# Kernel tuning notes

Measured on AMD Instinct MI355X. Metric: run time of the kernel, lower is better.

The kernel has to match this reference:

```python
import jax, jax.numpy as jnp
import numpy as np

B, L, D = 2, 2048, 1024
H = 16
DH = D // H
FACTOR = 0.6
U = max(1, min(L, int(FACTOR * L)))  # 1228 selected queries


def setup_inputs() -> dict:
    key = jax.random.key(0)
    ks = jax.random.split(key, 9)
    s = 0.02
    return {
        "x": jax.random.normal(ks[0], (B, L, D), dtype=jnp.float32),
        "Wq": jax.random.normal(ks[1], (D, D), dtype=jnp.float32) * s,
        "bq": jnp.zeros((D,), dtype=jnp.float32),
        "Wk": jax.random.normal(ks[2], (D, D), dtype=jnp.float32) * s,
        "bk": jnp.zeros((D,), dtype=jnp.float32),
        "Wv": jax.random.normal(ks[3], (D, D), dtype=jnp.float32) * s,
        "bv": jnp.zeros((D,), dtype=jnp.float32),
        "Wo": jax.random.normal(ks[4], (D, D), dtype=jnp.float32) * s,
        "bo": jnp.zeros((D,), dtype=jnp.float32),
    }


def _split_heads(x):
    b, l, d = x.shape
    return x.reshape(b, l, H, DH).transpose(0, 2, 1, 3)  # [b,h,l,dh]


def reference(x, Wq, bq, Wk, bk, Wv, bv, Wo, bo):
    b, l, _ = x.shape
    scale = 1.0 / jnp.sqrt(jnp.asarray(DH, dtype=x.dtype))

    q = _split_heads(x @ Wq + bq)  # [b,h,l,dh]
    k = _split_heads(x @ Wk + bk)
    v = _split_heads(x @ Wv + bv)

    # full scores for sparsity heuristic
    scores = jnp.einsum("bhqd,bhkd->bhqk", q, k) * scale  # [b,h,l,l]
    sparsity = scores.max(axis=-1) - scores.mean(axis=-1)  # [b,h,l]

    _, top_idx = jax.lax.top_k(sparsity, U)  # [b,h,U]

    # gather selected queries, attend only on those rows
    q_sel = jnp.take_along_axis(q, top_idx[..., None], axis=2)  # [b,h,U,dh]
    scores_sel = jnp.einsum("bhud,bhkd->bhuk", q_sel, k) * scale  # [b,h,U,l]
    attn = jax.nn.softmax(scores_sel, axis=-1)
    out_sel = jnp.einsum("bhuk,bhkd->bhud", attn, v)  # [b,h,U,dh]

    # scatter back into zero-initialized output
    bi = jnp.arange(b)[:, None, None]
    hi = jnp.arange(H)[None, :, None]
    out = jnp.zeros_like(q).at[bi, hi, top_idx].set(out_sel)  # [b,h,l,dh]

    out = out.transpose(0, 2, 1, 3).reshape(b, l, D)
    return out @ Wo + bo
```

## Files before the change

kernel.cpp:

```cpp
#include <hip/hip_runtime.h>
#include <math.h>
#include <stdint.h>

#define Bn 2
#define Ln 2048
#define Dn 1024
#define Hn 16
#define DHn 64
#define Un 1228
#define BHn (Bn*Hn)
#define SCALE 0.125f
#define WIN 32
#define WHALF 16
#define SXf 16.0f
#define SWf 256.0f
#define SQf 16.0f
#define SVf 16.0f
#define SPf 16.0f
#define ESC_PROJ (1.0f / 4096.0f)
#define ESC_OUT  (1.0f / 65536.0f)
#define PSC (SCALE / 256.0f)
#define QPS 88

typedef _Float16 f16;
typedef __attribute__((ext_vector_type(8))) _Float16 f16x8;
typedef __attribute__((ext_vector_type(4))) float f32x4;
struct h4s { f16 x, y, z, w; };

__device__ __forceinline__ void splitf16(float f, f16& hi, f16& lo) {
  hi = (f16)f;
  lo = (f16)(f - (float)hi);
}

__device__ __forceinline__ void gl_lds16(const void* g, void* l) {
  __builtin_amdgcn_global_load_lds(
      (const __attribute__((address_space(1))) void*)g,
      (__attribute__((address_space(3))) void*)l, 16, 0, 0);
}

#define MFMA(a, b, c) __builtin_amdgcn_mfma_f32_16x16x32_f16((a), (b), (c), 0, 0, 0)

__global__ __launch_bounds__(256) void split_kernel(
    const float* __restrict__ in, f16* __restrict__ oh, f16* __restrict__ ol, int n4) {
  int i = blockIdx.x * 256 + threadIdx.x;
  if (i >= n4) return;
  float4 v = ((const float4*)in)[i];
  h4s h, l;
  splitf16(v.x * SXf, h.x, l.x); splitf16(v.y * SXf, h.y, l.y);
  splitf16(v.z * SXf, h.z, l.z); splitf16(v.w * SXf, h.w, l.w);
  ((h4s*)oh)[i] = h; ((h4s*)ol)[i] = l;
}

__global__ __launch_bounds__(256) void tsplit_w4(
    const float* __restrict__ W0, const float* __restrict__ W1,
    const float* __restrict__ W2, const float* __restrict__ W3,
    f16* __restrict__ oh, f16* __restrict__ ol) {
  __shared__ float ts[64][65];
  const int t = threadIdx.x;
  const int r0 = blockIdx.x * 64, c0 = blockIdx.y * 64;
  const int z = blockIdx.z;
  const float* in = (z == 0) ? W0 : (z == 1) ? W1 : (z == 2) ? W2 : W3;
#pragma unroll
  for (int c = 0; c < 4; ++c) {
    int f = (c * 256 + t) * 4; int row = f >> 6, col = f & 63;
    float4 v = *(const float4*)&in[(size_t)(r0 + row) * Dn + c0 + col];
    ts[row][col] = v.x; ts[row][col + 1] = v.y; ts[row][col + 2] = v.z; ts[row][col + 3] = v.w;
  }
  __syncthreads();
#pragma unroll
  for (int c = 0; c < 4; ++c) {
    int f = (c * 256 + t) * 4; int crow = f >> 6, rcol = f & 63;
    h4s h, l;
    splitf16(ts[rcol + 0][crow] * SWf, h.x, l.x);
    splitf16(ts[rcol + 1][crow] * SWf, h.y, l.y);
    splitf16(ts[rcol + 2][crow] * SWf, h.z, l.z);
    splitf16(ts[rcol + 3][crow] * SWf, h.w, l.w);
    size_t o = (size_t)(z * 1024 + c0 + crow) * Dn + r0 + rcol;
    *(h4s*)&oh[o] = h; *(h4s*)&ol[o] = l;
  }
}

__global__ void gemm_qkv(
    const f16* __restrict__ Ah, const f16* __restrict__ Al,
    const f16* __restrict__ Bth, const f16* __restrict__ Btl,
    const float* __restrict__ bq, const float* __restrict__ bk, const float* __restrict__ bv,
    float* __restrict__ Qf, f16* __restrict__ Qbh,
    float* __restrict__ Kf, f16* __restrict__ Kbh,
    f16* __restrict__ Vh16, int K) {
  __shared__ f16 sAh[128 * 32], sAl[128 * 32], sBh[128 * 32], sBl[128 * 32];
  const int t = threadIdx.x;
  const int w = t >> 6, lane = t & 63, lm = lane & 15, q = lane >> 4;
  const int wr = w >> 1, wc = w & 1;
  const int n0 = blockIdx.x * 128, m0 = blockIdx.y * 128;
  f32x4 acc[4][4] = {};
  for (int k0 = 0; k0 < K; k0 += 32) {
    const f16* s0 = Ah + (size_t)m0 * K + k0;
    const f16* s1 = Al + (size_t)m0 * K + k0;
    const f16* s2 = Bth + (size_t)n0 * K + k0;
    const f16* s3 = Btl + (size_t)n0 * K + k0;
#pragma unroll
    for (int c = 0; c < 2; ++c) {
      int f = (c * 256 + t) * 8; int row = f >> 5, col = f & 31;
      size_t go = (size_t)row * K + col;
      gl_lds16(s0 + go, &sAh[f]);
      gl_lds16(s1 + go, &sAl[f]);
      gl_lds16(s2 + go, &sBh[f]);
      gl_lds16(s3 + go, &sBl[f]);
    }
    __syncthreads();
    f16x8 a_h[4], a_l[4], b_h[4], b_l[4];
#pragma unroll
    for (int mi = 0; mi < 4; ++mi) {
      int r = (wr * 64 + mi * 16 + lm) * 32 + q * 8;
      a_h[mi] = *(const f16x8*)&sAh[r];
      a_l[mi] = *(const f16x8*)&sAl[r];
    }
#pragma unroll
    for (int ni = 0; ni < 4; ++ni) {
      int r = (wc * 64 + ni * 16 + lm) * 32 + q * 8;
      b_h[ni] = *(const f16x8*)&sBh[r];
      b_l[ni] = *(const f16x8*)&sBl[r];
    }
#pragma unroll
    for (int mi = 0; mi < 4; ++mi)
#pragma unroll
      for (int ni = 0; ni < 4; ++ni) {
        acc[mi][ni] = MFMA(a_h[mi], b_h[ni], acc[mi][ni]);
        acc[mi][ni] = MFMA(a_h[mi], b_l[ni], acc[mi][ni]);
        acc[mi][ni] = MFMA(a_l[mi], b_h[ni], acc[mi][ni]);
      }
    __syncthreads();
  }
#pragma unroll
  for (int mi = 0; mi < 4; ++mi)
#pragma unroll
    for (int ni = 0; ni < 4; ++ni) {
      int nglob = n0 + wc * 64 + ni * 16;
      int seg = nglob >> 10;
      int c = (nglob & 1023) + lm;
      const float* bp = (seg == 0) ? bq : (seg == 1) ? bk : bv;
      float bvv = bp[c];
#pragma unroll
      for (int r = 0; r < 4; ++r) {
        int grow = m0 + wr * 64 + mi * 16 + q * 4 + r;
        float v = acc[mi][ni][r] * ESC_PROJ + bvv;
        size_t o = (size_t)grow * 1024 + c;
        if (seg == 0) {
          Qf[o] = v;
          Qbh[o] = (f16)(v * SQf);
        } else if (seg == 1) {
          Kf[o] = v;
          Kbh[o] = (f16)(v * SQf);
        } else {
          Vh16[o] = (f16)(v * SVf);
        }
      }
    }
}

__global__ __launch_bounds__(256) void tsplit_v(
    const f16* __restrict__ Vh16, f16* __restrict__ out) {
  __shared__ f16 ts[64][72];
  const int t = threadIdx.x;
  const int l0 = blockIdx.x * 64;
  const int bh = blockIdx.y, b = bh >> 4, h = bh & 15;
#pragma unroll
  for (int c = 0; c < 2; ++c) {
    int e = c * 256 + t; int row = e >> 3, cg = e & 7;
    *(uint4*)&ts[row][cg * 8] =
        *(const uint4*)&Vh16[((size_t)b * Ln + l0 + row) * Dn + h * DHn + cg * 8];
  }
  __syncthreads();
#pragma unroll
  for (int c = 0; c < 2; ++c) {
    int e = c * 256 + t; int drow = e >> 3, lg = e & 7;
    f16 tmp[8];
#pragma unroll
    for (int j = 0; j < 8; ++j) tmp[j] = ts[lg * 8 + j][drow];
    *(uint4*)&out[((size_t)bh * DHn + drow) * Ln + l0 + lg * 8] = *(uint4*)tmp;
  }
}

__global__ __launch_bounds__(256, 4) void gemm_a1(
    const f16* __restrict__ A,
    const f16* __restrict__ Bth, const f16* __restrict__ Btl,
    const float* __restrict__ bias, float escale,
    float* __restrict__ Cf, int M, int N, int K) {
  __shared__ f16 sA[128 * 32], sBh[64 * 32], sBl[64 * 32];
  const int t = threadIdx.x;
  const int w = t >> 6, lane = t & 63, lm = lane & 15, q = lane >> 4;
  const int wr = w >> 1, wc = w & 1;
  const int n0 = blockIdx.x * 64, m0 = blockIdx.y * 128;
  f32x4 acc[4][2] = {};
  for (int k0 = 0; k0 < K; k0 += 32) {
    const f16* s0 = A + (size_t)m0 * K + k0;
    const f16* s2 = Bth + (size_t)n0 * K + k0;
    const f16* s3 = Btl + (size_t)n0 * K + k0;
#pragma unroll
    for (int c = 0; c < 2; ++c) {
      int f = (c * 256 + t) * 8; int row = f >> 5, col = f & 31;
      gl_lds16(s0 + (size_t)row * K + col, &sA[f]);
    }
    {
      int f = t * 8; int row = f >> 5, col = f & 31;
      gl_lds16(s2 + (size_t)row * K + col, &sBh[f]);
      gl_lds16(s3 + (size_t)row * K + col, &sBl[f]);
    }
    __syncthreads();
    f16x8 a_[4], b_h[2], b_l[2];
#pragma unroll
    for (int mi = 0; mi < 4; ++mi)
      a_[mi] = *(const f16x8*)&sA[(wr * 64 + mi * 16 + lm) * 32 + q * 8];
#pragma unroll
    for (int ni = 0; ni < 2; ++ni) {
      int r = (wc * 32 + ni * 16 + lm) * 32 + q * 8;
      b_h[ni] = *(const f16x8*)&sBh[r];
      b_l[ni] = *(const f16x8*)&sBl[r];
    }
#pragma unroll
    for (int mi = 0; mi < 4; ++mi)
#pragma unroll
      for (int ni = 0; ni < 2; ++ni) {
        acc[mi][ni] = MFMA(a_[mi], b_h[ni], acc[mi][ni]);
        acc[mi][ni] = MFMA(a_[mi], b_l[ni], acc[mi][ni]);
      }
    __syncthreads();
  }
#pragma unroll
  for (int mi = 0; mi < 4; ++mi)
#pragma unroll
    for (int ni = 0; ni < 2; ++ni) {
      int gcol = n0 + wc * 32 + ni * 16 + lm;
      float bvv = bias[gcol];
#pragma unroll
      for (int r = 0; r < 4; ++r) {
        int grow = m0 + wr * 64 + mi * 16 + q * 4 + r;
        Cf[(size_t)grow * N + gcol] = acc[mi][ni][r] * escale + bvv;
      }
    }
}

__global__ __launch_bounds__(256) void ksum_part(
    const f16* __restrict__ Kh, float* __restrict__ ksum) {
  __shared__ float red[4][64];
  const int t = threadIdx.x, d = t & 63, seg = t >> 6;
  const int bx = blockIdx.x, bh = blockIdx.y, b = bh >> 4, h = bh & 15;
  float s = 0.f;
  const int lbase = bx * 256 + seg * 64;
  for (int r = 0; r < 64; ++r) {
    size_t o = ((size_t)b * Ln + lbase + r) * Dn + h * DHn + d;
    s += (float)Kh[o];
  }
  red[seg][d] = s;
  __syncthreads();
  if (t < 64) atomicAdd(&ksum[bh * DHn + t], red[0][t] + red[1][t] + red[2][t] + red[3][t]);
}

__global__ __launch_bounds__(256, 2) void attn_stats_mfma(
    const f16* __restrict__ Qh, const f16* __restrict__ Kh,
    const float* __restrict__ ksum,
    float* __restrict__ row_max, float* __restrict__ spars) {
  __shared__ f16 sQh[128 * 64], sKh[128 * 64];
  __shared__ float redm[128][5];
  const int t = threadIdx.x;
  const int w = t >> 6, lane = t & 63, lm = lane & 15, q = lane >> 4;
  const int bh = blockIdx.y, b = bh >> 4, h = bh & 15;
  const int q0 = blockIdx.x * 128;
  const f16* qsh = Qh + ((size_t)b * Ln + q0) * Dn + h * DHn;
#pragma unroll
  for (int c = 0; c < 4; ++c) {
    int f = (c * 256 + t) * 8; int row = f >> 6, c16 = (f >> 3) & 7;
    size_t go = (size_t)row * Dn + ((c16 ^ (row & 7)) << 3);
    gl_lds16(qsh + go, &sQh[f]);
  }
  __syncthreads();
  f16x8 a_h[8][2];
#pragma unroll
  for (int mi = 0; mi < 8; ++mi)
#pragma unroll
    for (int ks = 0; ks < 2; ++ks) {
      int row = mi * 16 + lm;
      int r = row * 64 + (((ks * 4 + q) ^ (row & 7)) << 3);
      a_h[mi][ks] = *(const f16x8*)&sQh[r];
    }
  float rmax[8][4];
#pragma unroll
  for (int mi = 0; mi < 8; ++mi)
#pragma unroll
    for (int r = 0; r < 4; ++r) rmax[mi][r] = -1e30f;

  for (int kt = 0; kt < Ln / 128; ++kt) {
    __syncthreads();
    const f16* ksh = Kh + ((size_t)b * Ln + kt * 128) * Dn + h * DHn;
#pragma unroll
    for (int c = 0; c < 4; ++c) {
      int f = (c * 256 + t) * 8; int row = f >> 6, c16 = (f >> 3) & 7;
      size_t go = (size_t)row * Dn + ((c16 ^ (row & 7)) << 3);
      gl_lds16(ksh + go, &sKh[f]);
    }
    __syncthreads();
#pragma unroll
    for (int ni = 0; ni < 2; ++ni) {
      int bcol = (w * 2 + ni) * 16;
      f16x8 b_h[2];
#pragma unroll
      for (int ks = 0; ks < 2; ++ks) {
        int row = bcol + lm;
        int r = row * 64 + (((ks * 4 + q) ^ (row & 7)) << 3);
        b_h[ks] = *(const f16x8*)&sKh[r];
      }
#pragma unroll
      for (int mi = 0; mi < 8; ++mi) {
        f32x4 acc = {0.f, 0.f, 0.f, 0.f};
        __builtin_amdgcn_s_setprio(1);
        acc = MFMA(a_h[mi][0], b_h[0], acc);
        acc = MFMA(a_h[mi][1], b_h[1], acc);
        __builtin_amdgcn_s_setprio(0);
#pragma unroll
        for (int r = 0; r < 4; ++r) rmax[mi][r] = fmaxf(rmax[mi][r], acc[r]);
      }
    }
  }
#pragma unroll
  for (int mi = 0; mi < 8; ++mi)
#pragma unroll
    for (int r = 0; r < 4; ++r) {
      float v = rmax[mi][r];
      v = fmaxf(v, __shfl_xor(v, 1)); v = fmaxf(v, __shfl_xor(v, 2));
      v = fmaxf(v, __shfl_xor(v, 4)); v = fmaxf(v, __shfl_xor(v, 8));
      if (lm == 0) redm[mi * 16 + q * 4 + r][w] = v;
    }
  __syncthreads();
  if (t < 128) {
    float m = fmaxf(fmaxf(redm[t][0], redm[t][1]), fmaxf(redm[t][2], redm[t][3]));
    float dot = 0.f;
    const float* kp = ksum + bh * DHn;
#pragma unroll
    for (int d = 0; d < 64; ++d) {
      int idx = t * 64 + ((((d >> 3) ^ (t & 7)) << 3) | (d & 7));
      dot += (float)sQh[idx] * kp[d];
    }
    row_max[(size_t)bh * Ln + q0 + t] = m * PSC;
    spars[(size_t)bh * Ln + q0 + t] = m * PSC - dot * (PSC / (float)Ln);
  }
}

__global__ __launch_bounds__(1024) void topk_sort(
    const float* __restrict__ spars, int* __restrict__ top_idx, int* __restrict__ wrow) {
  __shared__ unsigned long long keys[Ln];
  const int t = threadIdx.x;
  const int bh = blockIdx.x;
  for (int i = t; i < Ln; i += 1024) {
    unsigned u = __float_as_uint(spars[(size_t)bh * Ln + i]);
    u = (u & 0x80000000u) ? ~u : (u | 0x80000000u);
    u = ~u;
    keys[i] = ((unsigned long long)u << 32) | (unsigned)i;
  }
  __syncthreads();
  for (int k = 2; k <= Ln; k <<= 1) {
    for (int j = k >> 1; j > 0; j >>= 1) {
      int i = ((t & ~(j - 1)) << 1) | (t & (j - 1));
      int ixj = i | j;
      unsigned long long a = keys[i], bb = keys[ixj];
      bool up = ((i & k) == 0);
      if ((a > bb) == up) { keys[i] = bb; keys[ixj] = a; }
      __syncthreads();
    }
  }
  for (int u = t; u < Un - WHALF; u += 1024)
    top_idx[(size_t)bh * Un + u] = (int)(keys[u] & 0xFFFFFFFFu);
  if (t < WIN) wrow[bh * WIN + t] = (int)(keys[Un - WHALF + t] & 0xFFFFFFFFu);
}

__global__ __launch_bounds__(256) void refine_part(
    const float* __restrict__ Qf, const float* __restrict__ Kf,
    const int* __restrict__ wrow,
    float* __restrict__ pmaxf, float* __restrict__ psum) {
  __shared__ float qs[WIN][68];
  __shared__ float redm[4][WIN], reds[4][WIN];
  const int t = threadIdx.x;
  const int bx = blockIdx.x, bh = blockIdx.y, b = bh >> 4, h = bh & 15;
  {
    int j = t >> 3, d0 = (t & 7) * 8;
    int qi = wrow[bh * WIN + j];
    const float* qp = &Qf[((size_t)b * Ln + qi) * Dn + h * DHn + d0];
    *(float4*)&qs[j][d0] = *(const float4*)qp;
    *(float4*)&qs[j][d0 + 4] = *(const float4*)(qp + 4);
  }
  __syncthreads();
  const int ki = bx * 256 + t;
  const float* kp = &Kf[((size_t)b * Ln + ki) * Dn + h * DHn];
  float s[WIN];
#pragma unroll
  for (int j = 0; j < WIN; ++j) s[j] = 0.f;
#pragma unroll 4
  for (int d0 = 0; d0 < 64; d0 += 4) {
    float4 k4 = *(const float4*)&kp[d0];
#pragma unroll
    for (int j = 0; j < WIN; ++j) {
      float4 q4 = *(const float4*)&qs[j][d0];
      s[j] = fmaf(k4.x, q4.x, s[j]);
      s[j] = fmaf(k4.y, q4.y, s[j]);
      s[j] = fmaf(k4.z, q4.z, s[j]);
      s[j] = fmaf(k4.w, q4.w, s[j]);
    }
  }
  const int w = t >> 6, lane = t & 63;
#pragma unroll
  for (int j = 0; j < WIN; ++j) {
    float mx = s[j], sm = s[j];
#pragma unroll
    for (int off = 1; off < 64; off <<= 1) {
      mx = fmaxf(mx, __shfl_xor(mx, off));
      sm += __shfl_xor(sm, off);
    }
    if (lane == 0) { redm[w][j] = mx; reds[w][j] = sm; }
  }
  __syncthreads();
  if (t < WIN) {
    float mx = fmaxf(fmaxf(redm[0][t], redm[1][t]), fmaxf(redm[2][t], redm[3][t]));
    float sm = reds[0][t] + reds[1][t] + reds[2][t] + reds[3][t];
    size_t o = ((size_t)bh * WIN + t) * 8 + bx;
    pmaxf[o] = mx;
    psum[o] = sm;
  }
}

__global__ __launch_bounds__(64) void topk_final(
    const float* __restrict__ pmaxf, const float* __restrict__ psum,
    const int* __restrict__ wrow, int* __restrict__ top_idx) {
  __shared__ float spxL[WIN];
  const int bh = blockIdx.x;
  const int t = threadIdx.x;
  if (t < WIN) {
    float m = -1e30f, s = 0.f;
#pragma unroll
    for (int p = 0; p < 8; ++p) {
      size_t o = ((size_t)bh * WIN + t) * 8 + p;
      m = fmaxf(m, pmaxf[o]);
      s += psum[o];
    }
    spxL[t] = SCALE * (m - s * (1.0f / (float)Ln));
  }
  __syncthreads();
  if (t != 0) return;
  float v[WIN]; int r[WIN];
#pragma unroll
  for (int j = 0; j < WIN; ++j) { v[j] = spxL[j]; r[j] = wrow[bh * WIN + j]; }
  unsigned taken = 0;
  for (int s2 = 0; s2 < WHALF; ++s2) {
    int best = -1;
    for (int j = 0; j < WIN; ++j) {
      if (taken & (1u << j)) continue;
      if (best < 0 || v[j] > v[best] || (v[j] == v[best] && r[j] < r[best])) best = j;
    }
    taken |= 1u << best;
    top_idx[(size_t)bh * Un + (Un - WHALF) + s2] = r[best];
  }
}

__global__ __launch_bounds__(256, 4) void attn_sel_part(
    const f16* __restrict__ Qh, const f16* __restrict__ Kh,
    const f16* __restrict__ Vth,
    const int* __restrict__ topi, const float* __restrict__ row_max,
    float* __restrict__ pO, float* __restrict__ pD) {
  __shared__ f16 sK[64 * 64], sV[64 * 64];
  __shared__ f16 sQP[64 * QPS];
  __shared__ float rmL[64];
  __shared__ int qxL[64];
  __shared__ float dred[64][5];
  const int t = threadIdx.x;
  const int w = t >> 6, lane = t & 63, lm = lane & 15, q = lane >> 4;
  const int half = blockIdx.y & 1, bh = blockIdx.y >> 1, b = bh >> 4, h = bh & 15;
  const int u0 = blockIdx.x * 64;
  const int nrows = (Un - u0 < 64) ? (Un - u0) : 64;
  if (t < 64) {
    int qi = topi[(size_t)bh * Un + ((t < nrows) ? (u0 + t) : 0)];
    qxL[t] = qi;
    rmL[t] = row_max[(size_t)bh * Ln + qi];
  }
  __syncthreads();
#pragma unroll
  for (int c = 0; c < 2; ++c) {
    int f = (c * 256 + t) * 8; int row = f >> 6, col = f & 63;
    size_t go = ((size_t)b * Ln + qxL[row]) * Dn + h * DHn + col;
    *(uint4*)&sQP[row * QPS + col] = *(const uint4*)&Qh[go];
  }
  __syncthreads();
  f16x8 aq[4][2];
#pragma unroll
  for (int mi = 0; mi < 4; ++mi)
#pragma unroll
    for (int ks = 0; ks < 2; ++ks)
      aq[mi][ks] = *(const f16x8*)&sQP[(mi * 16 + lm) * QPS + ks * 32 + q * 8];
  f32x4 oacc[4] = {};
  float dacc[4][4] = {};

  const f16* kbase = Kh + (size_t)b * Ln * Dn + h * DHn;
  const f16* vbase = Vth + (size_t)bh * DHn * Ln;
  for (int kt = 0; kt < 16; ++kt) {
    const int l0 = half * 1024 + kt * 64;
    __syncthreads();
#pragma unroll
    for (int c = 0; c < 2; ++c) {
      int f = (c * 256 + t) * 8; int row = f >> 6, c16 = (f >> 3) & 7;
      int sc = (c16 ^ (row & 7)) << 3;
      gl_lds16(kbase + (size_t)(l0 + row) * Dn + sc, &sK[f]);
      gl_lds16(vbase + (size_t)row * Ln + l0 + sc, &sV[f]);
    }
    __syncthreads();
    f16x8 kb[2];
#pragma unroll
    for (int ks = 0; ks < 2; ++ks) {
      int row = w * 16 + lm;
      kb[ks] = *(const f16x8*)&sK[row * 64 + (((ks * 4 + q) ^ (row & 7)) << 3)];
    }
#pragma unroll
    for (int mi = 0; mi < 4; ++mi) {
      f32x4 acc = {0.f, 0.f, 0.f, 0.f};
      __builtin_amdgcn_s_setprio(1);
      acc = MFMA(aq[mi][0], kb[0], acc);
      acc = MFMA(aq[mi][1], kb[1], acc);
      __builtin_amdgcn_s_setprio(0);
#pragma unroll
      for (int r = 0; r < 4; ++r) {
        int row = mi * 16 + q * 4 + r;
        float p = __expf(acc[r] * PSC - rmL[row]);
        dacc[mi][r] += p;
        sQP[row * QPS + w * 16 + lm] = (f16)(p * SPf);
      }
    }
    __syncthreads();
    f16x8 vb[2];
#pragma unroll
    for (int ks = 0; ks < 2; ++ks) {
      int row = w * 16 + lm;
      vb[ks] = *(const f16x8*)&sV[row * 64 + (((ks * 4 + q) ^ (row & 7)) << 3)];
    }
#pragma unroll
    for (int mi = 0; mi < 4; ++mi) {
      f16x8 pf0 = *(const f16x8*)&sQP[(mi * 16 + lm) * QPS + 0 * 32 + q * 8];
      f16x8 pf1 = *(const f16x8*)&sQP[(mi * 16 + lm) * QPS + 1 * 32 + q * 8];
      __builtin_amdgcn_s_setprio(1);
      oacc[mi] = MFMA(pf0, vb[0], oacc[mi]);
      oacc[mi] = MFMA(pf1, vb[1], oacc[mi]);
      __builtin_amdgcn_s_setprio(0);
    }
  }
#pragma unroll
  for (int mi = 0; mi < 4; ++mi)
#pragma unroll
    for (int r = 0; r < 4; ++r) {
      float v = dacc[mi][r];
      v += __shfl_xor(v, 1); v += __shfl_xor(v, 2);
      v += __shfl_xor(v, 4); v += __shfl_xor(v, 8);
      if (lm == 0) dred[mi * 16 + q * 4 + r][w] = v;
    }
  __syncthreads();
  const size_t pbase = ((size_t)half * BHn + bh) * 1280 + u0;
  if (t < 64)
    pD[pbase + t] = dred[t][0] + dred[t][1] + dred[t][2] + dred[t][3];
#pragma unroll
  for (int mi = 0; mi < 4; ++mi)
#pragma unroll
    for (int r = 0; r < 4; ++r) {
      int row = mi * 16 + q * 4 + r;
      pO[(pbase + row) * 64 + w * 16 + lm] = oacc[mi][r];
    }
}

__global__ __launch_bounds__(256) void attn_combine(
    const float* __restrict__ pO, const float* __restrict__ pD,
    const int* __restrict__ topi, f16* __restrict__ AOh) {
  const int t = threadIdx.x;
  const int u0 = blockIdx.x * 64, bh = blockIdx.y, b = bh >> 4, h = bh & 15;
  const int nrows = (Un - u0 < 64) ? (Un - u0) : 64;
  const int row = t >> 2, pg = t & 3;
  if (row >= nrows) return;
  int qi = topi[(size_t)bh * Un + u0 + row];
  size_t i0 = (size_t)bh * 1280 + u0 + row;
  size_t i1 = (size_t)BHn * 1280 + i0;
  float dinv = 1.0f / (pD[i0] + pD[i1]);
  const float* p0 = &pO[i0 * 64 + pg * 16];
  const float* p1 = &pO[i1 * 64 + pg * 16];
  f16 buf[16];
#pragma unroll
  for (int c = 0; c < 4; ++c) {
    float4 a = *(const float4*)&p0[c * 4];
    float4 bb = *(const float4*)&p1[c * 4];
    buf[c * 4 + 0] = (f16)((a.x + bb.x) * dinv);
    buf[c * 4 + 1] = (f16)((a.y + bb.y) * dinv);
    buf[c * 4 + 2] = (f16)((a.z + bb.z) * dinv);
    buf[c * 4 + 3] = (f16)((a.w + bb.w) * dinv);
  }
  f16* dst = &AOh[((size_t)b * Ln + qi) * Dn + h * DHn + pg * 16];
  *(uint4*)&dst[0] = *(uint4*)&buf[0];
  *(uint4*)&dst[8] = *(uint4*)&buf[8];
}

extern "C" void kernel_launch(void* const* d_in, const int* in_sizes, int n_in,
                              void* d_out, int out_size, void* d_ws, size_t ws_size,
                              hipStream_t stream) {
  (void)in_sizes; (void)n_in; (void)out_size; (void)ws_size;
  const float* x  = (const float*)d_in[0];
  const float* Wq = (const float*)d_in[1];
  const float* bq = (const float*)d_in[2];
  const float* Wk = (const float*)d_in[3];
  const float* bk = (const float*)d_in[4];
  const float* Wv = (const float*)d_in[5];
  const float* bv = (const float*)d_in[6];
  const float* Wo = (const float*)d_in[7];
  const float* bo = (const float*)d_in[8];
  float* out = (float*)d_out;

  uint8_t* p = (uint8_t*)d_ws;
  const size_t NE = (size_t)Bn * Ln * Dn;
  f16* xh = (f16*)p;  p += NE * 2;
  f16* xl = (f16*)p;  p += NE * 2;
  f16* Wt_h = (f16*)p; p += (size_t)4096 * Dn * 2;
  f16* Wt_l = (f16*)p; p += (size_t)4096 * Dn * 2;
  f16* Qbh = (f16*)p; p += NE * 2;
  f16* Kbh = (f16*)p; p += NE * 2;
  float* Qf = (float*)p;  p += NE * 4;
  float* Kf = (float*)p;  p += NE * 4;
  f16* Vh16 = (f16*)p; p += NE * 2;
  f16* Vth  = (f16*)p; p += NE * 2;
  float* rowmax = (float*)p; p += (size_t)BHn * Ln * 4;
  float* spars  = (float*)p; p += (size_t)BHn * Ln * 4;
  float* ksum   = (float*)p; p += (size_t)BHn * DHn * 4;
  int* topi     = (int*)p;   p += (size_t)BHn * Un * 4;
  int* wrow     = (int*)p;   p += (size_t)BHn * WIN * 4;
  float* pmaxf  = (float*)p; p += (size_t)BHn * WIN * 8 * 4;
  float* psum   = (float*)p; p += (size_t)BHn * WIN * 8 * 4;
  float* pD     = (float*)p; p += (size_t)2 * BHn * 1280 * 4;
  float* pO = Qf;
  f16* AOh = xh;

  dim3 blk(256);
  hipLaunchKernelGGL(split_kernel, dim3((int)(NE / 4 / 256)), blk, 0, stream, x, xh, xl, (int)(NE / 4));
  hipLaunchKernelGGL(tsplit_w4, dim3(16, 16, 4), blk, 0, stream, Wq, Wk, Wv, Wo, Wt_h, Wt_l);
  hipLaunchKernelGGL(gemm_qkv, dim3(24, 32), blk, 0, stream, xh, xl, Wt_h, Wt_l,
                     bq, bk, bv, Qf, Qbh, Kf, Kbh, Vh16, Dn);
  hipLaunchKernelGGL(tsplit_v, dim3(Ln / 64, BHn), blk, 0, stream, Vh16, Vth);
  hipMemsetAsync(ksum, 0, (size_t)BHn * DHn * 4, stream);
  hipLaunchKernelGGL(ksum_part, dim3(8, BHn), blk, 0, stream, Kbh, ksum);
  hipLaunchKernelGGL(attn_stats_mfma, dim3(Ln / 128, BHn), blk, 0, stream,
                     Qbh, Kbh, ksum, rowmax, spars);
  hipLaunchKernelGGL(topk_sort, dim3(BHn), dim3(1024), 0, stream, spars, topi, wrow);
  hipLaunchKernelGGL(refine_part, dim3(8, BHn), blk, 0, stream, Qf, Kf, wrow, pmaxf, psum);
  hipLaunchKernelGGL(topk_final, dim3(BHn), dim3(64), 0, stream, pmaxf, psum, wrow, topi);
  hipMemsetAsync(AOh, 0, NE * 2, stream);
  hipLaunchKernelGGL(attn_sel_part, dim3((Un + 63) / 64, 2 * BHn), blk, 0, stream,
                     Qbh, Kbh, Vth, topi, rowmax, pO, pD);
  hipLaunchKernelGGL(attn_combine, dim3((Un + 63) / 64, BHn), blk, 0, stream,
                     pO, pD, topi, AOh);
  hipLaunchKernelGGL(gemm_a1, dim3(16, 32), blk, 0, stream, AOh,
                     Wt_h + (size_t)3072 * Dn, Wt_l + (size_t)3072 * Dn, bo,
                     ESC_OUT, out, Bn * Ln, Dn, Dn);
}
```

Baseline: 384.0 us.

## Double-buffer attention K/V, remap GEMM blocks, store Q/K as split fp16

The selected-query attention kernel now double-buffers its K/V tiles in LDS, prefetching the next tile while computing the current one, and the launch-bounds occupancy hint drops to fit the larger LDS footprint. Both GEMMs use a 1D grid with a swizzled block-to-tile mapping meant to improve cache locality across CUs. Q and K are no longer written as fp32 copies. They are stored as hi/lo fp16 pairs, which cuts write bandwidth, and refine_part reconstructs fp32 from these pairs. pO gets its own buffer instead of aliasing Qf, adding workspace memory.

```diff
diff --git a/kernel.cpp b/kernel.cpp
--- a/kernel.cpp
+++ b/kernel.cpp
@@ -84,14 +84,17 @@
     const f16* __restrict__ Ah, const f16* __restrict__ Al,
     const f16* __restrict__ Bth, const f16* __restrict__ Btl,
     const float* __restrict__ bq, const float* __restrict__ bk, const float* __restrict__ bv,
-    float* __restrict__ Qf, f16* __restrict__ Qbh,
-    float* __restrict__ Kf, f16* __restrict__ Kbh,
+    f16* __restrict__ Qbh, f16* __restrict__ Qbl,
+    f16* __restrict__ Kbh, f16* __restrict__ Kbl,
     f16* __restrict__ Vh16, int K) {
   __shared__ f16 sAh[128 * 32], sAl[128 * 32], sBh[128 * 32], sBl[128 * 32];
   const int t = threadIdx.x;
   const int w = t >> 6, lane = t & 63, lm = lane & 15, q = lane >> 4;
   const int wr = w >> 1, wc = w & 1;
-  const int n0 = blockIdx.x * 128, m0 = blockIdx.y * 128;
+  int ob = blockIdx.x;
+  int wg = (ob & 7) * 96 + (ob >> 3);
+  const int bx = wg % 24, by = wg / 24;
+  const int n0 = bx * 128, m0 = by * 128;
   f32x4 acc[4][4] = {};
   for (int k0 = 0; k0 < K; k0 += 32) {
     const f16* s0 = Ah + (size_t)m0 * K + k0;
@@ -146,11 +149,9 @@
         float v = acc[mi][ni][r] * ESC_PROJ + bvv;
         size_t o = (size_t)grow * 1024 + c;
         if (seg == 0) {
-          Qf[o] = v;
-          Qbh[o] = (f16)(v * SQf);
+          f16 hh, ll; splitf16(v * SQf, hh, ll); Qbh[o] = hh; Qbl[o] = ll;
         } else if (seg == 1) {
-          Kf[o] = v;
-          Kbh[o] = (f16)(v * SQf);
+          f16 hh, ll; splitf16(v * SQf, hh, ll); Kbh[o] = hh; Kbl[o] = ll;
         } else {
           Vh16[o] = (f16)(v * SVf);
         }
@@ -190,7 +191,9 @@
   const int t = threadIdx.x;
   const int w = t >> 6, lane = t & 63, lm = lane & 15, q = lane >> 4;
   const int wr = w >> 1, wc = w & 1;
-  const int n0 = blockIdx.x * 64, m0 = blockIdx.y * 128;
+  int ob = blockIdx.x;
+  int wg = (ob & 7) * 64 + (ob >> 3);
+  const int n0 = (wg & 15) * 64, m0 = (wg >> 4) * 128;
   f32x4 acc[4][2] = {};
   for (int k0 = 0; k0 < K; k0 += 32) {
     const f16* s0 = A + (size_t)m0 * K + k0;
@@ -373,7 +376,8 @@
 }
 
 __global__ __launch_bounds__(256) void refine_part(
-    const float* __restrict__ Qf, const float* __restrict__ Kf,
+    const f16* __restrict__ Qbh, const f16* __restrict__ Qbl,
+    const f16* __restrict__ Kbh, const f16* __restrict__ Kbl,
     const int* __restrict__ wrow,
     float* __restrict__ pmaxf, float* __restrict__ psum) {
   __shared__ float qs[WIN][68];
@@ -383,27 +387,29 @@
   {
     int j = t >> 3, d0 = (t & 7) * 8;
     int qi = wrow[bh * WIN + j];
-    const float* qp = &Qf[((size_t)b * Ln + qi) * Dn + h * DHn + d0];
-    *(float4*)&qs[j][d0] = *(const float4*)qp;
-    *(float4*)&qs[j][d0 + 4] = *(const float4*)(qp + 4);
+    size_t o = ((size_t)b * Ln + qi) * Dn + h * DHn + d0;
+    f16x8 vh = *(const f16x8*)&Qbh[o];
+    f16x8 vl = *(const f16x8*)&Qbl[o];
+#pragma unroll
+    for (int e = 0; e < 8; ++e) qs[j][d0 + e] = (float)vh[e] + (float)vl[e];
   }
   __syncthreads();
   const int ki = bx * 256 + t;
-  const float* kp = &Kf[((size_t)b * Ln + ki) * Dn + h * DHn];
+  const size_t ko = ((size_t)b * Ln + ki) * Dn + h * DHn;
   float s[WIN];
 #pragma unroll
   for (int j = 0; j < WIN; ++j) s[j] = 0.f;
-#pragma unroll 4
-  for (int d0 = 0; d0 < 64; d0 += 4) {
-    float4 k4 = *(const float4*)&kp[d0];
-#pragma unroll
-    for (int j = 0; j < WIN; ++j) {
-      float4 q4 = *(const float4*)&qs[j][d0];
-      s[j] = fmaf(k4.x, q4.x, s[j]);
-      s[j] = fmaf(k4.y, q4.y, s[j]);
-      s[j] = fmaf(k4.z, q4.z, s[j]);
-      s[j] = fmaf(k4.w, q4.w, s[j]);
-    }
+  for (int d0 = 0; d0 < 64; d0 += 8) {
+    f16x8 vh = *(const f16x8*)&Kbh[ko + d0];
+    f16x8 vl = *(const f16x8*)&Kbl[ko + d0];
+    float kf[8];
+#pragma unroll
+    for (int e = 0; e < 8; ++e) kf[e] = (float)vh[e] + (float)vl[e];
+#pragma unroll
+    for (int e = 0; e < 8; ++e)
+#pragma unroll
+      for (int j = 0; j < WIN; ++j)
+        s[j] = fmaf(kf[e], qs[j][d0 + e], s[j]);
   }
   const int w = t >> 6, lane = t & 63;
 #pragma unroll
@@ -440,7 +446,7 @@
       m = fmaxf(m, pmaxf[o]);
       s += psum[o];
     }
-    spxL[t] = SCALE * (m - s * (1.0f / (float)Ln));
+    spxL[t] = PSC * (m - s * (1.0f / (float)Ln));
   }
   __syncthreads();
   if (t != 0) return;
@@ -459,12 +465,12 @@
   }
 }
 
-__global__ __launch_bounds__(256, 4) void attn_sel_part(
+__global__ __launch_bounds__(256, 3) void attn_sel_part(
     const f16* __restrict__ Qh, const f16* __restrict__ Kh,
     const f16* __restrict__ Vth,
     const int* __restrict__ topi, const float* __restrict__ row_max,
     float* __restrict__ pO, float* __restrict__ pD) {
-  __shared__ f16 sK[64 * 64], sV[64 * 64];
+  __shared__ f16 sK[2][64 * 64], sV[2][64 * 64];
   __shared__ f16 sQP[64 * QPS];
   __shared__ float rmL[64];
   __shared__ int qxL[64];
@@ -498,22 +504,37 @@
 
   const f16* kbase = Kh + (size_t)b * Ln * Dn + h * DHn;
   const f16* vbase = Vth + (size_t)bh * DHn * Ln;
-  for (int kt = 0; kt < 16; ++kt) {
-    const int l0 = half * 1024 + kt * 64;
-    __syncthreads();
+
+  {
+    const int l0 = half * 1024;
 #pragma unroll
     for (int c = 0; c < 2; ++c) {
       int f = (c * 256 + t) * 8; int row = f >> 6, c16 = (f >> 3) & 7;
       int sc = (c16 ^ (row & 7)) << 3;
-      gl_lds16(kbase + (size_t)(l0 + row) * Dn + sc, &sK[f]);
-      gl_lds16(vbase + (size_t)row * Ln + l0 + sc, &sV[f]);
-    }
-    __syncthreads();
+      gl_lds16(kbase + (size_t)(l0 + row) * Dn + sc, &sK[0][f]);
+      gl_lds16(vbase + (size_t)row * Ln + l0 + sc, &sV[0][f]);
+    }
+  }
+  asm volatile("s_waitcnt vmcnt(0) lgkmcnt(0)" ::: "memory");
+  __builtin_amdgcn_s_barrier();
+
+  for (int kt = 0; kt < 16; ++kt) {
+    const int cur = kt & 1;
     f16x8 kb[2];
 #pragma unroll
     for (int ks = 0; ks < 2; ++ks) {
       int row = w * 16 + lm;
-      kb[ks] = *(const f16x8*)&sK[row * 64 + (((ks * 4 + q) ^ (row & 7)) << 3)];
+      kb[ks] = *(const f16x8*)&sK[cur][row * 64 + (((ks * 4 + q) ^ (row & 7)) << 3)];
+    }
+    if (kt < 15) {
+      const int ln0 = half * 1024 + (kt + 1) * 64;
+#pragma unroll
+      for (int c = 0; c < 2; ++c) {
+        int f = (c * 256 + t) * 8; int row = f >> 6, c16 = (f >> 3) & 7;
+        int sc = (c16 ^ (row & 7)) << 3;
+        gl_lds16(kbase + (size_t)(ln0 + row) * Dn + sc, &sK[cur ^ 1][f]);
+        gl_lds16(vbase + (size_t)row * Ln + ln0 + sc, &sV[cur ^ 1][f]);
+      }
     }
 #pragma unroll
     for (int mi = 0; mi < 4; ++mi) {
@@ -530,12 +551,13 @@
         sQP[row * QPS + w * 16 + lm] = (f16)(p * SPf);
       }
     }
-    __syncthreads();
+    asm volatile("s_waitcnt lgkmcnt(0)" ::: "memory");
+    __builtin_amdgcn_s_barrier();
     f16x8 vb[2];
 #pragma unroll
     for (int ks = 0; ks < 2; ++ks) {
       int row = w * 16 + lm;
-      vb[ks] = *(const f16x8*)&sV[row * 64 + (((ks * 4 + q) ^ (row & 7)) << 3)];
+      vb[ks] = *(const f16x8*)&sV[cur][row * 64 + (((ks * 4 + q) ^ (row & 7)) << 3)];
     }
 #pragma unroll
     for (int mi = 0; mi < 4; ++mi) {
@@ -546,6 +568,8 @@
       oacc[mi] = MFMA(pf1, vb[1], oacc[mi]);
       __builtin_amdgcn_s_setprio(0);
     }
+    asm volatile("s_waitcnt vmcnt(0)" ::: "memory");
+    __builtin_amdgcn_s_barrier();
   }
 #pragma unroll
   for (int mi = 0; mi < 4; ++mi)
@@ -620,9 +644,9 @@
   f16* Wt_h = (f16*)p; p += (size_t)4096 * Dn * 2;
   f16* Wt_l = (f16*)p; p += (size_t)4096 * Dn * 2;
   f16* Qbh = (f16*)p; p += NE * 2;
+  f16* Qbl = (f16*)p; p += NE * 2;
   f16* Kbh = (f16*)p; p += NE * 2;
-  float* Qf = (float*)p;  p += NE * 4;
-  float* Kf = (float*)p;  p += NE * 4;
+  f16* Kbl = (f16*)p; p += NE * 2;
   f16* Vh16 = (f16*)p; p += NE * 2;
   f16* Vth  = (f16*)p; p += NE * 2;
   float* rowmax = (float*)p; p += (size_t)BHn * Ln * 4;
@@ -633,28 +657,29 @@
   float* pmaxf  = (float*)p; p += (size_t)BHn * WIN * 8 * 4;
   float* psum   = (float*)p; p += (size_t)BHn * WIN * 8 * 4;
   float* pD     = (float*)p; p += (size_t)2 * BHn * 1280 * 4;
-  float* pO = Qf;
+  float* pO     = (float*)p; p += (size_t)2 * BHn * 1280 * 64 * 4;
   f16* AOh = xh;
 
   dim3 blk(256);
   hipLaunchKernelGGL(split_kernel, dim3((int)(NE / 4 / 256)), blk, 0, stream, x, xh, xl, (int)(NE / 4));
   hipLaunchKernelGGL(tsplit_w4, dim3(16, 16, 4), blk, 0, stream, Wq, Wk, Wv, Wo, Wt_h, Wt_l);
-  hipLaunchKernelGGL(gemm_qkv, dim3(24, 32), blk, 0, stream, xh, xl, Wt_h, Wt_l,
-                     bq, bk, bv, Qf, Qbh, Kf, Kbh, Vh16, Dn);
+  hipLaunchKernelGGL(gemm_qkv, dim3(768), blk, 0, stream, xh, xl, Wt_h, Wt_l,
+                     bq, bk, bv, Qbh, Qbl, Kbh, Kbl, Vh16, Dn);
   hipLaunchKernelGGL(tsplit_v, dim3(Ln / 64, BHn), blk, 0, stream, Vh16, Vth);
   hipMemsetAsync(ksum, 0, (size_t)BHn * DHn * 4, stream);
   hipLaunchKernelGGL(ksum_part, dim3(8, BHn), blk, 0, stream, Kbh, ksum);
   hipLaunchKernelGGL(attn_stats_mfma, dim3(Ln / 128, BHn), blk, 0, stream,
                      Qbh, Kbh, ksum, rowmax, spars);
   hipLaunchKernelGGL(topk_sort, dim3(BHn), dim3(1024), 0, stream, spars, topi, wrow);
-  hipLaunchKernelGGL(refine_part, dim3(8, BHn), blk, 0, stream, Qf, Kf, wrow, pmaxf, psum);
+  hipLaunchKernelGGL(refine_part, dim3(8, BHn), blk, 0, stream,
+                     Qbh, Qbl, Kbh, Kbl, wrow, pmaxf, psum);
   hipLaunchKernelGGL(topk_final, dim3(BHn), dim3(64), 0, stream, pmaxf, psum, wrow, topi);
   hipMemsetAsync(AOh, 0, NE * 2, stream);
   hipLaunchKernelGGL(attn_sel_part, dim3((Un + 63) / 64, 2 * BHn), blk, 0, stream,
                      Qbh, Kbh, Vth, topi, rowmax, pO, pD);
   hipLaunchKernelGGL(attn_combine, dim3((Un + 63) / 64, BHn), blk, 0, stream,
                      pO, pD, topi, AOh);
-  hipLaunchKernelGGL(gemm_a1, dim3(16, 32), blk, 0, stream, AOh,
+  hipLaunchKernelGGL(gemm_a1, dim3(512), blk, 0, stream, AOh,
                      Wt_h + (size_t)3072 * Dn, Wt_l + (size_t)3072 * Dn, bo,
                      ESC_OUT, out, Bn * Ln, Dn, Dn);
 }
```

Result: faster. 376.2 us (-2.0%).
